# Performance work log

Hardware: AMD Instinct MI355X
Metric: run time of the kernel (lower is better)

The kernel has to match this reference:

```python
import jax, jax.numpy as jnp
import numpy as np


def _component_indices(d, j):
    # Butterfly component at level j has block size k = d >> j.
    k = d >> j
    half = k // 2
    base = np.arange(d // k) * k                       # block starts
    p = (base[:, None] + np.arange(half)[None, :]).reshape(-1)  # [d//2]
    q = p + half
    return p, q


def butterfly_rotation(thetas, d):
    """Compose m = log2(d) butterfly components: R = B(d,d) @ B(d,d/2) @ ... @ B(d,2).
    thetas: [m, d//2] Givens angles per component (block-major order as in torch)."""
    m = thetas.shape[0]
    R = jnp.eye(d, dtype=thetas.dtype)
    for j in range(m):
        p, q = _component_indices(d, j)
        c = jnp.cos(thetas[j])
        s = jnp.sin(thetas[j])
        C = jnp.eye(d, dtype=thetas.dtype)
        C = C.at[p, p].set(c)
        C = C.at[q, q].set(c)
        C = C.at[p, q].set(-s)
        C = C.at[q, p].set(s)
        R = R @ C
    return R


def setup_inputs() -> dict:
    key = jax.random.key(0)
    ks = jax.random.split(key, 8)
    N, D_IN, D_OUT, R = 16384, 4096, 4096, 1024
    M = 10  # log2(R)
    return {
        "x": jax.random.normal(ks[0], (N, D_IN), dtype=jnp.float32),
        "W": jax.random.normal(ks[1], (D_OUT, D_IN), dtype=jnp.float32) * 0.02,
        "bias": jax.random.normal(ks[2], (D_OUT,), dtype=jnp.float32) * 0.02,
        "U": jax.random.normal(ks[3], (D_OUT, R), dtype=jnp.float32) * 0.02,
        "S": jax.random.uniform(ks[4], (R,), dtype=jnp.float32),
        "V": jax.random.normal(ks[5], (R, D_IN), dtype=jnp.float32) * 0.02,
        "thetas_u": jax.random.normal(ks[6], (M, R // 2), dtype=jnp.float32) * 0.1,
        "thetas_v": jax.random.normal(ks[7], (M, R // 2), dtype=jnp.float32) * 0.1,
    }


def reference(x, W, bias, U, S, V, thetas_u, thetas_v):
    r = S.shape[0]
    R_U = butterfly_rotation(thetas_u, r)  # [r, r]
    R_V = butterfly_rotation(thetas_v, r)  # [r, r]
    # base_layer(x)
    base = x @ W.T + bias                  # [N, out]
    # adapter: x @ V^T @ R_V @ diag(S) @ R_U^T @ U^T
    h = (x @ V.T) @ R_V                    # [N, r]
    h = h * S                              # diag(S)
    delta = (h @ R_U.T) @ U.T              # [N, out]
    return base + delta
```

## Files before the change

### kernel.cpp

```cpp
#include <hip/hip_runtime.h>
#include <cstdint>
#include <cstddef>


typedef __bf16 bf16x8 __attribute__((ext_vector_type(8)));
typedef float floatx4 __attribute__((ext_vector_type(4)));
typedef unsigned short ushortx8 __attribute__((ext_vector_type(8)));

__device__ __forceinline__ unsigned short f2bf(float f) {
    unsigned int u = __builtin_bit_cast(unsigned int, f);
    u += 0x7FFFu + ((u >> 16) & 1u);
    return (unsigned short)(u >> 16);
}

__device__ __forceinline__ void gld_lds16(const void* g, void* l) {
    __builtin_amdgcn_global_load_lds(
        (const __attribute__((address_space(1))) void*)g,
        (__attribute__((address_space(3))) void*)l,
        16, 0, 0);
}

__device__ __forceinline__ bf16x8 ldsv(const char* p) {
    return __builtin_bit_cast(bf16x8, *(const ushortx8*)p);
}

#define MFMA_BF16(a, b, c) __builtin_amdgcn_mfma_f32_16x16x32_bf16((a), (b), (c), 0, 0, 0)
#define SCHED0() __builtin_amdgcn_sched_barrier(0)

__global__ __launch_bounds__(256) void butterfly_rows_kernel(
    const float* __restrict__ thetas_v, const float* __restrict__ thetas_u,
    const float* __restrict__ S,
    unsigned short* __restrict__ RVsb, unsigned short* __restrict__ RUb)
{
    const int d = 1024;
    __shared__ float w[1024];
    const int b   = blockIdx.x;
    const int mat = b >> 10;
    const int row = b & 1023;
    const float* th = mat ? thetas_u : thetas_v;
    const int t = threadIdx.x;

    for (int i = t; i < d; i += 256) w[i] = (i == row) ? 1.f : 0.f;
    __syncthreads();

    for (int j = 0; j < 10; ++j) {
        const int sh = 9 - j;
        const int halfm1 = (1 << sh) - 1;
        for (int i = t; i < d / 2; i += 256) {
            const int blk = i >> sh;
            const int off = i & halfm1;
            const int p = (blk << (sh + 1)) + off;
            const int q = p + (halfm1 + 1);
            const float theta = th[j * (d / 2) + i];
            float s, c;
            __sincosf(theta, &s, &c);
            const float wp = w[p], wq = w[q];
            w[p] = c * wp + s * wq;
            w[q] = -s * wp + c * wq;
        }
        __syncthreads();
    }

    if (mat == 0) {
        for (int i = t; i < d; i += 256) RVsb[row * d + i] = f2bf(w[i] * S[i]);
    } else {
        for (int i = t; i < d; i += 256) RUb[row * d + i] = f2bf(w[i]);
    }
}

__global__ __launch_bounds__(256) void cvt_f32_bf16_x8(
    const float* __restrict__ src, unsigned short* __restrict__ dst)
{
    const size_t i = ((size_t)blockIdx.x * 256 + threadIdx.x) * 8;
    float4 a = *(const float4*)(src + i);
    float4 b = *(const float4*)(src + i + 4);
    ushortx8 o;
    o[0] = f2bf(a.x); o[1] = f2bf(a.y); o[2] = f2bf(a.z); o[3] = f2bf(a.w);
    o[4] = f2bf(b.x); o[5] = f2bf(b.y); o[6] = f2bf(b.z); o[7] = f2bf(b.w);
    *(ushortx8*)(dst + i) = o;
}

__global__ __launch_bounds__(256) void transpose_to_bf16(
    const float* __restrict__ src, unsigned short* __restrict__ dst,
    int rows, int cols)
{
    __shared__ float tile[32][33];
    const int tx = threadIdx.x & 31, ty = threadIdx.x >> 5;
    const int c0 = blockIdx.x * 32, r0 = blockIdx.y * 32;
    for (int i = 0; i < 32; i += 8)
        tile[ty + i][tx] = src[(size_t)(r0 + ty + i) * cols + c0 + tx];
    __syncthreads();
    for (int i = 0; i < 32; i += 8)
        dst[(size_t)(c0 + ty + i) * rows + r0 + tx] = f2bf(tile[tx][ty + i]);
}

template <int EPI>
__global__ __launch_bounds__(256) void gemm_nt(
    const unsigned short* __restrict__ A,
    const unsigned short* __restrict__ B,
    float* __restrict__ Cf,
    unsigned short* __restrict__ Cb,
    const float* __restrict__ extra,
    int M, int N, int K)
{
    __shared__ __align__(16) unsigned short As[128 * 32];
    __shared__ __align__(16) unsigned short Bs[128 * 32];

    const int tid  = threadIdx.x;
    const int lane = tid & 63;
    const int wave = tid >> 6;
    const int wm = wave >> 1, wn = wave & 1;

    const int m0 = blockIdx.y * 128;
    const int n0 = blockIdx.x * 128;

    const int srow = wave * 32 + (lane >> 2);
    const int scol = (lane & 3) * 8;

    const unsigned short* gA = A + (size_t)(m0 + srow) * K + scol;
    const unsigned short* gB = B + (size_t)(n0 + srow) * K + scol;
    unsigned short* lA = As + wave * 32 * 32;
    unsigned short* lB = Bs + wave * 32 * 32;

    floatx4 acc[4][4];
#pragma unroll
    for (int i = 0; i < 4; ++i)
#pragma unroll
        for (int j = 0; j < 4; ++j) acc[i][j] = (floatx4)0.f;

    const int ar = lane & 15;
    const int ak = (lane >> 4) * 8;

    for (int kk = 0; kk < K; kk += 32) {
        gld_lds16(gA + kk, lA);
        gld_lds16(gA + kk + (size_t)16 * K, lA + 512);
        gld_lds16(gB + kk, lB);
        gld_lds16(gB + kk + (size_t)16 * K, lB + 512);
        __syncthreads();

        bf16x8 af[4], bfr[4];
#pragma unroll
        for (int tm = 0; tm < 4; ++tm)
            af[tm] = __builtin_bit_cast(bf16x8,
                *(const ushortx8*)&As[(wm * 64 + tm * 16 + ar) * 32 + ak]);
#pragma unroll
        for (int tn = 0; tn < 4; ++tn)
            bfr[tn] = __builtin_bit_cast(bf16x8,
                *(const ushortx8*)&Bs[(wn * 64 + tn * 16 + ar) * 32 + ak]);
#pragma unroll
        for (int tm = 0; tm < 4; ++tm)
#pragma unroll
            for (int tn = 0; tn < 4; ++tn)
                acc[tm][tn] = MFMA_BF16(af[tm], bfr[tn], acc[tm][tn]);
        __syncthreads();
    }

#pragma unroll
    for (int tm = 0; tm < 4; ++tm) {
#pragma unroll
        for (int tn = 0; tn < 4; ++tn) {
#pragma unroll
            for (int r = 0; r < 4; ++r) {
                const int row = m0 + wm * 64 + tm * 16 + (lane >> 4) * 4 + r;
                const int col = n0 + wn * 64 + tn * 16 + (lane & 15);
                const float v = acc[tm][tn][r];
                if (EPI == 1) {
                    Cf[(size_t)row * N + col] = v + extra[col];
                } else if (EPI == 2) {
                    Cb[(size_t)row * N + col] = f2bf(v);
                } else {
                    Cb[(size_t)row * N + col] = f2bf(v + extra[(size_t)row * N + col]);
                }
            }
        }
    }
}

#define RD_AF0() do { _Pragma("unroll") \
    for (int mf = 0; mf < 4; ++mf) { \
        af0[mf][0] = ldsv(Ad + arb + mf * 2048 + ca0); \
        af0[mf][1] = ldsv(Ad + arb + mf * 2048 + ca1); } } while (0)
#define RD_AF1() do { _Pragma("unroll") \
    for (int mf = 0; mf < 4; ++mf) { \
        af1[mf][0] = ldsv(Ad + 16384 + arb + mf * 2048 + ca0); \
        af1[mf][1] = ldsv(Ad + 16384 + arb + mf * 2048 + ca1); } } while (0)
#define RD_B0() do { _Pragma("unroll") \
    for (int nf = 0; nf < 2; ++nf) { \
        b0[nf][0] = ldsv(Bd + brb + nf * 2048 + ca0); \
        b0[nf][1] = ldsv(Bd + brb + nf * 2048 + ca1); } } while (0)
#define RD_B1() do { _Pragma("unroll") \
    for (int nf = 0; nf < 2; ++nf) { \
        b1[nf][0] = ldsv(Bd + 16384 + brb + nf * 2048 + ca0); \
        b1[nf][1] = ldsv(Bd + 16384 + brb + nf * 2048 + ca1); } } while (0)
#define MMQ(A_, B_, mo, no) do { \
    __builtin_amdgcn_s_setprio(1); \
    _Pragma("unroll") \
    for (int mf = 0; mf < 4; ++mf) \
        _Pragma("unroll") \
        for (int nf = 0; nf < 2; ++nf) { \
            acc[(mo) + mf][(no) + nf] = MFMA_BF16(A_[mf][0], B_[nf][0], acc[(mo) + mf][(no) + nf]); \
            acc[(mo) + mf][(no) + nf] = MFMA_BF16(A_[mf][1], B_[nf][1], acc[(mo) + mf][(no) + nf]); } \
    __builtin_amdgcn_s_setprio(0); } while (0)

template <int EPI>
__global__ __launch_bounds__(512, 2) void gemm256(
    const unsigned short* __restrict__ A,
    const unsigned short* __restrict__ B,
    float* __restrict__ Cf,
    unsigned short* __restrict__ Cb,
    const float* __restrict__ extra,
    int M, int N, int K, int swz_on)
{
    __shared__ __align__(16) unsigned short As[2][2][128][64];
    __shared__ __align__(16) unsigned short Bs[2][2][128][64];

    const int tid  = threadIdx.x;
    const int lane = tid & 63;
    const int wave = tid >> 6;
    const int wm = wave >> 2;
    const int wn = wave & 3;

    int bx = blockIdx.x, by = blockIdx.y;
    if (swz_on) {
        const int gx  = gridDim.x;
        const int nwg = gx * gridDim.y;
        const int f   = by * gx + bx;
        const int g   = (f & 7) * (nwg >> 3) + (f >> 3);
        bx = g % gx;
        by = g / gx;
    }
    const int m0 = by * 256;
    const int n0 = bx * 256;

    const int srow  = tid >> 3;
    const int scolb = (tid & 7) << 4;
    const int scol  = (scolb ^ ((srow & 7) << 4)) >> 1;
    const unsigned short* gA = A + (size_t)(m0 + srow) * K + scol;
    const unsigned short* gB = B + (size_t)(n0 + srow) * K + scol;
    char* lA = (char*)As + (wave << 10);
    char* lB = (char*)Bs + (wave << 10);
    const size_t rs64 = (size_t)64 * K;

    auto stA = [&](int src_t, int dbuf, int h) {
        const unsigned short* s = gA + (size_t)h * 2 * rs64 + (size_t)src_t * 64;
        char* l = lA + dbuf * 32768 + h * 16384;
        gld_lds16(s, l);
        gld_lds16(s + rs64, l + 8192);
    };
    auto stB = [&](int src_t, int dbuf, int h) {
        const unsigned short* s = gB + (size_t)h * 2 * rs64 + (size_t)src_t * 64;
        char* l = lB + dbuf * 32768 + h * 16384;
        gld_lds16(s, l);
        gld_lds16(s + rs64, l + 8192);
    };

    const int fr  = lane & 15;
    const int kg  = lane >> 4;
    const int swz = (fr & 7) << 4;
    const int ca0 = (kg << 4) ^ swz;
    const int ca1 = (64 + (kg << 4)) ^ swz;
    const int arb = (wm * 64 + fr) * 128;
    const int brb = (wn * 32 + fr) * 128;

    floatx4 acc[8][4];
#pragma unroll
    for (int i = 0; i < 8; ++i)
#pragma unroll
        for (int j = 0; j < 4; ++j) acc[i][j] = (floatx4)0.f;

    const int nkt = K >> 6;

    stA(0, 0, 0); stB(0, 0, 0); stB(0, 0, 1); stA(0, 0, 1);

    for (int t = 0; t < nkt; ++t) {
        const int cb = t & 1, nb = cb ^ 1;
        const char* Ad = (const char*)As + cb * 32768;
        const char* Bd = (const char*)Bs + cb * 32768;

        __builtin_amdgcn_s_barrier();
        if (t + 1 < nkt) {
            stA(t + 1, nb, 0); stB(t + 1, nb, 0);
            stB(t + 1, nb, 1); stA(t + 1, nb, 1);
            asm volatile("s_waitcnt vmcnt(8)" ::: "memory");
        } else {
            asm volatile("s_waitcnt vmcnt(0)" ::: "memory");
        }
        SCHED0();

        bf16x8 af0[4][2], af1[4][2], b0[2][2], b1[2][2];

        if ((wave & 1) == 0) {
            RD_AF0(); RD_B0();
            MMQ(af0, b0, 0, 0);
            RD_B1();
            MMQ(af0, b1, 0, 2);
            RD_AF1();
            MMQ(af1, b1, 4, 2);
            MMQ(af1, b0, 4, 0);
        } else {
            RD_AF1(); RD_B1();
            MMQ(af1, b1, 4, 2);
            RD_B0();
            MMQ(af1, b0, 4, 0);
            RD_AF0();
            MMQ(af0, b0, 0, 0);
            MMQ(af0, b1, 0, 2);
        }
    }

    const int er4 = (lane >> 4) << 2;
    const int ec  = lane & 15;
#pragma unroll
    for (int Mq = 0; Mq < 2; ++Mq)
#pragma unroll
        for (int mf = 0; mf < 4; ++mf)
#pragma unroll
            for (int Nq = 0; Nq < 2; ++Nq)
#pragma unroll
                for (int nf = 0; nf < 2; ++nf)
#pragma unroll
                    for (int r = 0; r < 4; ++r) {
                        const int row = m0 + Mq * 128 + wm * 64 + mf * 16 + er4 + r;
                        const int col = n0 + Nq * 128 + wn * 32 + nf * 16 + ec;
                        const float v = acc[Mq * 4 + mf][Nq * 2 + nf][r];
                        if (EPI == 1) {
                            Cf[(size_t)row * N + col] = v + extra[col];
                        } else {
                            Cb[(size_t)row * N + col] = f2bf(v + extra[(size_t)row * N + col]);
                        }
                    }
    (void)M;
}

extern "C" void kernel_launch(void* const* d_in, const int* in_sizes, int n_in,
                              void* d_out, int out_size, void* d_ws, size_t ws_size,
                              hipStream_t stream)
{
    const int NB = 16384, DIN = 4096, DOUT = 4096, R = 1024;

    const float* x    = (const float*)d_in[0];
    const float* W    = (const float*)d_in[1];
    const float* bias = (const float*)d_in[2];
    const float* U    = (const float*)d_in[3];
    const float* S    = (const float*)d_in[4];
    const float* V    = (const float*)d_in[5];
    const float* th_u = (const float*)d_in[6];
    const float* th_v = (const float*)d_in[7];
    float* out = (float*)d_out;

    char* ws = (char*)d_ws;
    size_t off = 0;
    auto alloc = [&](size_t bytes) {
        char* p = ws + off;
        off += (bytes + 255) & ~(size_t)255;
        return p;
    };
    unsigned short* Xb   = (unsigned short*)alloc((size_t)NB * DIN * 2);
    unsigned short* Wctb = (unsigned short*)alloc((size_t)DOUT * DIN * 2);
    unsigned short* RVsb = (unsigned short*)alloc((size_t)R * R * 2);
    unsigned short* RUb  = (unsigned short*)alloc((size_t)R * R * 2);
    unsigned short* Tb   = (unsigned short*)alloc((size_t)R * R * 2);
    unsigned short* Ub   = (unsigned short*)alloc((size_t)DOUT * R * 2);
    unsigned short* Gb   = (unsigned short*)alloc((size_t)DOUT * R * 2);
    unsigned short* Vtb  = (unsigned short*)alloc((size_t)DIN * R * 2);
    if (off > ws_size) return;

    butterfly_rows_kernel<<<2048, 256, 0, stream>>>(th_v, th_u, S, RVsb, RUb);

    cvt_f32_bf16_x8<<<(NB * (size_t)DIN) / 2048, 256, 0, stream>>>(x, Xb);
    cvt_f32_bf16_x8<<<((size_t)DOUT * R) / 2048, 256, 0, stream>>>(U, Ub);
    transpose_to_bf16<<<dim3(DIN / 32, R / 32), 256, 0, stream>>>(V, Vtb, R, DIN);

    gemm_nt<2><<<dim3(R / 128, R / 128), 256, 0, stream>>>(
        RVsb, RUb, nullptr, Tb, nullptr, R, R, R);

    gemm_nt<2><<<dim3(R / 128, DOUT / 128), 256, 0, stream>>>(
        Ub, Tb, nullptr, Gb, nullptr, DOUT, R, R);

    gemm256<3><<<dim3(DIN / 256, DOUT / 256), 512, 0, stream>>>(
        Gb, Vtb, nullptr, Wctb, W, DOUT, DIN, R, 0);

    gemm256<1><<<dim3(DOUT / 256, NB / 256), 512, 0, stream>>>(
        Xb, Wctb, out, nullptr, bias, NB, DOUT, DIN, 1);
}
```

Baseline: 1.233 ms.

## Interleave global-to-LDS prefetch with MFMA quadrants using barrier-synchronized ping-pong schedule

```diff
diff --git a/kernel.cpp b/kernel.cpp
--- a/kernel.cpp
+++ b/kernel.cpp
@@ -271,41 +271,63 @@
     const int nkt = K >> 6;
 
     stA(0, 0, 0); stB(0, 0, 0); stB(0, 0, 1); stA(0, 0, 1);
+    asm volatile("s_waitcnt vmcnt(4)" ::: "memory");
+    stA(1, 1, 0); stB(1, 1, 0); stB(1, 1, 1);
+    asm volatile("s_waitcnt vmcnt(6)" ::: "memory");
+    SCHED0();
+    __builtin_amdgcn_s_barrier();
+    SCHED0();
 
     for (int t = 0; t < nkt; ++t) {
         const int cb = t & 1, nb = cb ^ 1;
         const char* Ad = (const char*)As + cb * 32768;
         const char* Bd = (const char*)Bs + cb * 32768;
 
-        __builtin_amdgcn_s_barrier();
-        if (t + 1 < nkt) {
-            stA(t + 1, nb, 0); stB(t + 1, nb, 0);
-            stB(t + 1, nb, 1); stA(t + 1, nb, 1);
-            asm volatile("s_waitcnt vmcnt(8)" ::: "memory");
-        } else {
+        bf16x8 af0[4][2], af1[4][2], b0[2][2], b1[2][2];
+
+        RD_AF0(); RD_B0();
+        if (t + 1 < nkt) stA(t + 1, nb, 1);
+        asm volatile("s_waitcnt lgkmcnt(8)" ::: "memory");
+        SCHED0();
+        __builtin_amdgcn_s_barrier();
+        asm volatile("s_waitcnt lgkmcnt(0)" ::: "memory");
+        SCHED0();
+        MMQ(af0, b0, 0, 0);
+        SCHED0();
+        __builtin_amdgcn_s_barrier();
+
+        RD_B1();
+        if (t + 2 < nkt) stA(t + 2, cb, 0);
+        SCHED0();
+        __builtin_amdgcn_s_barrier();
+        asm volatile("s_waitcnt lgkmcnt(0)" ::: "memory");
+        SCHED0();
+        MMQ(af0, b1, 0, 2);
+        SCHED0();
+        __builtin_amdgcn_s_barrier();
+
+        RD_AF1();
+        if (t + 2 < nkt) stB(t + 2, cb, 0);
+        SCHED0();
+        __builtin_amdgcn_s_barrier();
+        asm volatile("s_waitcnt lgkmcnt(0)" ::: "memory");
+        SCHED0();
+        MMQ(af1, b1, 4, 2);
+        SCHED0();
+        __builtin_amdgcn_s_barrier();
+
+        if (t + 2 < nkt) stB(t + 2, cb, 1);
+        if (t == nkt - 2) {
             asm volatile("s_waitcnt vmcnt(0)" ::: "memory");
+        } else if (t < nkt - 2) {
+            asm volatile("s_waitcnt vmcnt(6)" ::: "memory");
         }
         SCHED0();
-
-        bf16x8 af0[4][2], af1[4][2], b0[2][2], b1[2][2];
-
-        if ((wave & 1) == 0) {
-            RD_AF0(); RD_B0();
-            MMQ(af0, b0, 0, 0);
-            RD_B1();
-            MMQ(af0, b1, 0, 2);
-            RD_AF1();
-            MMQ(af1, b1, 4, 2);
-            MMQ(af1, b0, 4, 0);
-        } else {
-            RD_AF1(); RD_B1();
-            MMQ(af1, b1, 4, 2);
-            RD_B0();
-            MMQ(af1, b0, 4, 0);
-            RD_AF0();
-            MMQ(af0, b0, 0, 0);
-            MMQ(af0, b1, 0, 2);
-        }
+        __builtin_amdgcn_s_barrier();
+        SCHED0();
+        MMQ(af1, b0, 4, 0);
+        SCHED0();
+        __builtin_amdgcn_s_barrier();
     }
 
     const int er4 = (lane >> 4) << 2;
```

Measured after the change: 1.075 ms. -12.9%, faster.
